# Kernel optimization log

Hardware: AMD Instinct MI355X
Metric: run time of the kernel (lower is better)

## Reference

```python
import jax, jax.numpy as jnp
import numpy as np
from jax.scipy.linalg import expm

T, N, M_IN, DT = 8192, 1024, 512, 0.01


def setup_inputs() -> dict:
    key = jax.random.key(0)
    kA, kB, ky, ku = jax.random.split(key, 4)
    ts = jnp.arange(T, dtype=jnp.float32) * DT
    # Mildly stable dynamics so the trajectory stays bounded over T steps.
    A = 0.1 * jax.random.normal(kA, (N, N), jnp.float32) / np.sqrt(N) - 0.5 * jnp.eye(N, dtype=jnp.float32)
    B = jax.random.normal(kB, (N, M_IN), jnp.float32) / np.sqrt(M_IN)
    y0 = jax.random.normal(ky, (N,), jnp.float32)
    u = jax.random.normal(ku, (T, M_IN), jnp.float32)
    return {"ts": ts, "y0": y0, "u": u, "A": A, "B": B}


def reference(ts, y0, u, A, B):
    # Exact solution of dy/dt = A y + B u(t) with u piecewise-linear on ts
    # (what diffrax Tsit5+PID approximates to rtol=1e-3). Uses Van Loan's
    # augmented matrix exponential: z = [y; u; v] with u' = v, v' = 0.
    n = A.shape[0]
    m = B.shape[1]
    h = ts[1] - ts[0]  # uniform grid
    Z_nm = jnp.zeros((n, m), A.dtype)
    Mblk = jnp.block([
        [A, B, Z_nm],
        [jnp.zeros((m, n + m), A.dtype), jnp.eye(m, dtype=A.dtype)],
        [jnp.zeros((m, n + 2 * m), A.dtype)],
    ])
    E = expm(Mblk * h)
    Eyy = E[:n, :n]            # state transition e^{Ah}
    Eyu = E[:n, n:n + m]       # response to constant input u_k
    Eyv = E[:n, n + m:]        # response to input slope v_k
    v = (u[1:] - u[:-1]) / h                     # [T-1, m] slopes
    c = u[:-1] @ Eyu.T + v @ Eyv.T               # [T-1, n] affine terms

    def step(y, ck):
        y_next = Eyy @ y + ck
        return y_next, y_next

    _, ys = jax.lax.scan(step, y0, c)
    return jnp.concatenate([y0[None, :], ys], axis=0)  # [T, n]
```

## Files before the change

### kernel.cpp

```cpp
#include <hip/hip_runtime.h>

#define GT 8192
#define GN 1024
#define GM 512
#define CCH 1024
#define SCH 8

typedef __attribute__((ext_vector_type(8))) short bf16x8;
typedef __attribute__((ext_vector_type(4))) float f32x4;

__device__ __forceinline__ unsigned short f2bf(float x) {
    unsigned int u = __float_as_uint(x);
    u += 0x7FFF + ((u >> 16) & 1);
    return (unsigned short)(u >> 16);
}
__device__ __forceinline__ float bf2f(unsigned short b) {
    return __uint_as_float(((unsigned int)b) << 16);
}
__device__ __forceinline__ void split2(float x, unsigned short& h0, unsigned short& h1) {
    h0 = f2bf(x);
    h1 = f2bf(x - bf2f(h0));
}
__device__ __forceinline__ void split3(float x, unsigned short& s0,
                                       unsigned short& s1, unsigned short& s2) {
    s0 = f2bf(x); float r = x - bf2f(s0);
    s1 = f2bf(r); r -= bf2f(s1);
    s2 = f2bf(r);
}
__device__ __forceinline__ long swz(long e, int sh) {
    return e ^ (((e >> (sh + 1)) & 3) << 3);
}
__device__ __forceinline__ void gl16(const unsigned short* g, unsigned short* l) {
    __builtin_amdgcn_global_load_lds(
        (const __attribute__((address_space(1))) unsigned int*)g,
        (__attribute__((address_space(3))) unsigned int*)l, 16, 0, 0);
}

template <int BM, int WN, int KS>
__global__ __launch_bounds__(512) void gemm_pp(
    const unsigned short* __restrict__ Ap, long apsz, int alda, int aldsh,
    int amask, int ashift, int ashiftN,
    const unsigned short* __restrict__ Bp, long bpsz, long bstride,
    const float* __restrict__ Cf, long cfb, long cfld,
    const unsigned short* __restrict__ Cp, long cpsz, int cmask,
    int bzero, int bsplit, float beta, float betaB,
    float* __restrict__ Of, long ofb, long ofld, long ofstep,
    unsigned short* __restrict__ Pout, long ppsz, int pstep8, int pmode, int prowstep,
    int segN, int zoff, int trmask,
    int M, float alpha, float alphaB, int asplit, int add_id,
    const unsigned short* __restrict__ Ap2, long apsz2,
    const unsigned short* __restrict__ Bp2,
    unsigned short* __restrict__ Pout2, long ppsz2, int p2off, int seg2,
    unsigned short* __restrict__ PoutT, int tposeN)
{
    constexpr int NQ = 2 * WN;
    constexpr int MTM = BM / 32;
    constexpr int MTN = BM / (WN * 16);
    constexpr int CPW = KS * BM / 32;
    __shared__ __align__(16) unsigned short At[2][KS][2][BM][32];
    __shared__ __align__(16) unsigned short Bt[2][KS][2][BM][32];

    const int tid = threadIdx.x;
    const int lane = tid & 63;
    const int w = tid >> 6;
    const int ksub = w / NQ;
    const int quad = w % NQ;
    const int wr = (quad / WN) * (BM / 2);
    const int wc = (quad % WN) * (BM / WN);
    const int l16 = lane & 15, koff = lane >> 4;
    const int row0 = blockIdx.x * BM;
    const int col0 = blockIdx.y * BM;
    const int lr4 = lane >> 2;
    const int lg = lane & 3;
    const bool s2 = (Ap2 != nullptr) && (row0 >= seg2);
    const bool lead = (KS == 1) || (ksub == 0);
    const int segk = row0 >> 10;

    f32x4 acc[MTM][MTN] = {};

    auto stage = [&](int bsel, int k0) {
        #pragma unroll
        for (int ci = 0; ci < CPW; ++ci) {
            const int c = w * CPW + ci;
            const int op = c / (KS * BM / 8);
            const int rem = c % (KS * BM / 8);
            const int limb = rem / (KS * BM / 16);
            const int rem2 = rem % (KS * BM / 16);
            const int kk = rem2 / (BM / 16);
            const int rb = (rem2 % (BM / 16)) * 16;
            const int lr = rb + lr4;
            const int q = lg ^ ((lr >> 1) & 3);
            long e; int sh; const unsigned short* base;
            if (op == 0) {
                if (!s2) {
                    int ar = (row0 + lr) & amask;
                    if (ar < ashiftN) { ar -= ashift; if (ar < 0) ar = 0; }
                    e = (long)ar * alda + k0 + kk * 32 + (q << 3); sh = aldsh;
                    base = Ap + (limb ? apsz : 0);
                } else {
                    e = (long)(row0 - seg2 + lr) * 1024 + k0 + kk * 32 + (q << 3); sh = 10;
                    base = Ap2 + (limb ? apsz2 : 0);
                }
            } else {
                e = (long)(col0 + lr) * 1024 + k0 + kk * 32 + (q << 3); sh = 10;
                base = (s2 ? Bp2 : (Bp + (long)segk * bstride)) + (limb ? bpsz : 0);
            }
            long f = swz(e, sh);
            unsigned short* l = (op == 0 ? &At[bsel][kk][limb][rb][0]
                                         : &Bt[bsel][kk][limb][rb][0]);
            gl16(base + f, l);
        }
    };

    stage(0, 0);
    __syncthreads();
    int cur = 0;
    for (int k0 = 0; k0 < 1024; k0 += KS * 32) {
        if (k0 + KS * 32 < 1024) stage(cur ^ 1, k0 + KS * 32);

        const int kk = ksub;
        bf16x8 a0[MTM], a1[MTM], b0[MTN], b1[MTN];
        #pragma unroll
        for (int mi = 0; mi < MTM; ++mi) {
            int lr = wr + mi * 16 + l16;
            int off = (koff ^ ((lr >> 1) & 3)) << 3;
            a0[mi] = *(const bf16x8*)&At[cur][kk][0][lr][off];
            a1[mi] = *(const bf16x8*)&At[cur][kk][1][lr][off];
        }
        #pragma unroll
        for (int ni = 0; ni < MTN; ++ni) {
            int lr = wc + ni * 16 + l16;
            int off = (koff ^ ((lr >> 1) & 3)) << 3;
            b0[ni] = *(const bf16x8*)&Bt[cur][kk][0][lr][off];
            b1[ni] = *(const bf16x8*)&Bt[cur][kk][1][lr][off];
        }
        #pragma unroll
        for (int mi = 0; mi < MTM; ++mi)
            #pragma unroll
            for (int ni = 0; ni < MTN; ++ni) {
                f32x4 cc = acc[mi][ni];
                cc = __builtin_amdgcn_mfma_f32_16x16x32_bf16(a0[mi], b0[ni], cc, 0, 0, 0);
                cc = __builtin_amdgcn_mfma_f32_16x16x32_bf16(a0[mi], b1[ni], cc, 0, 0, 0);
                cc = __builtin_amdgcn_mfma_f32_16x16x32_bf16(a1[mi], b0[ni], cc, 0, 0, 0);
                acc[mi][ni] = cc;
            }
        __syncthreads();
        cur ^= 1;
    }

    if (KS == 2) {
        float* red = (float*)&At[0][0][0][0][0];
        if (ksub == 1) {
            #pragma unroll
            for (int mi = 0; mi < MTM; ++mi)
                #pragma unroll
                for (int ni = 0; ni < MTN; ++ni)
                    *(f32x4*)&red[(((quad * MTM + mi) * MTN + ni) * 64 + lane) * 4] =
                        acc[mi][ni];
        }
        __syncthreads();
        if (ksub == 0) {
            #pragma unroll
            for (int mi = 0; mi < MTM; ++mi)
                #pragma unroll
                for (int ni = 0; ni < MTN; ++ni) {
                    f32x4 o = *(const f32x4*)
                        &red[(((quad * MTM + mi) * MTN + ni) * 64 + lane) * 4];
                    acc[mi][ni][0] += o[0]; acc[mi][ni][1] += o[1];
                    acc[mi][ni][2] += o[2]; acc[mi][ni][3] += o[3];
                }
        }
    }

    const bool tp = (PoutT != nullptr) && (row0 >= tposeN);
    float* T = (float*)&Bt[0][0][0][0][0];

    if (s2) {
        if (lead) {
            #pragma unroll
            for (int mi = 0; mi < MTM; ++mi)
                #pragma unroll
                for (int r = 0; r < 4; ++r) {
                    const int gr = row0 + wr + mi * 16 + koff * 4 + r;
                    if (gr >= M) continue;
                    const int prow = gr - seg2 + p2off;
                    #pragma unroll
                    for (int ni = 0; ni < MTN; ++ni) {
                        const int gc = col0 + wc + ni * 16 + l16;
                        float pv = acc[mi][ni][r];
                        if (Pout2) {
                            long f = swz((long)prow * 1024 + gc, 10);
                            unsigned short h0 = f2bf(pv);
                            Pout2[f] = h0;
                            Pout2[ppsz2 + f] = f2bf(pv - bf2f(h0));
                        }
                        if (tp) T[(wr + mi * 16 + koff * 4 + r) * 65 + gc - col0] = pv;
                    }
                }
        }
    } else {
        if (lead) {
            const long ofe = ofb + (long)segk * ofstep;
            const long cfe = cfb + (long)segk * ofstep;
            #pragma unroll
            for (int mi = 0; mi < MTM; ++mi) {
                #pragma unroll
                for (int r = 0; r < 4; ++r) {
                    const int gr = row0 + wr + mi * 16 + koff * 4 + r;
                    if (gr >= M) continue;
                    const int trow = (((gr < segN) ? gr + zoff : gr)) & trmask;
                    if (gr < segN && trow >= segN) continue;
                    const float aa = (trow < asplit) ? alpha : alphaB;
                    const float bb = (trow < bzero) ? 0.f
                                    : ((trow < bsplit) ? beta : betaB);
                    #pragma unroll
                    for (int ni = 0; ni < MTN; ++ni) {
                        const int gc = col0 + wc + ni * 16 + l16;
                        float vp = aa * acc[mi][ni][r];
                        float v = vp;
                        if (bb != 0.f) {
                            int crow = trow & cmask;
                            if (Cf) v += bb * Cf[cfe + (long)crow * cfld + gc];
                            else if (Cp) {
                                long f = swz((long)crow * 1024 + gc, 10);
                                v += bb * (bf2f(Cp[f]) + bf2f(Cp[cpsz + f]));
                            }
                        }
                        if (add_id && gr == gc) v += 1.f;
                        if (Of) Of[ofe + (long)trow * ofld + gc] = v;
                        if (Pout && (!pstep8 || (trow & 7) == 0)) {
                            int prow = (pstep8 ? (trow >> 3) : trow) + segk * prowstep;
                            long f = swz((long)prow * 1024 + gc, 10);
                            float pv = (pmode == 2) ? vp : v;
                            unsigned short h0 = f2bf(pv);
                            Pout[f] = h0;
                            Pout[ppsz + f] = f2bf(pv - bf2f(h0));
                        }
                        if (tp) T[(wr + mi * 16 + koff * 4 + r) * 65 + gc - col0] = v;
                    }
                }
            }
        }
    }

    if (BM == 64 && tp) {
        __syncthreads();
        if (tid < 256) {
            const int i = tid >> 2;
            const int jb = (tid & 3) * 16;
            const int prow = col0 + i;
            #pragma unroll
            for (int e2 = 0; e2 < 16; ++e2) {
                int j = jb + e2;
                float v = T[j * 65 + i];
                long f = swz((long)prow * 1024 + (row0 - tposeN + j), 10);
                unsigned short h0 = f2bf(v);
                PoutT[f] = h0;
                PoutT[(long)(1 << 20) + f] = f2bf(v - bf2f(h0));
            }
        }
    }
}

__global__ void split_pl_k(const float* __restrict__ X, unsigned short* __restrict__ P,
                           long psz, int ldsh, float s, long cnt)
{
    long i = (long)blockIdx.x * 256 + threadIdx.x;
    if (i >= cnt) return;
    float v = s * X[i];
    long f = swz(i, ldsh);
    unsigned short h0 = f2bf(v);
    P[f] = h0;
    P[psz + f] = f2bf(v - bf2f(h0));
}

__global__ void trsp_k(const float* __restrict__ in, int R, float s, int add_id,
                       unsigned short* __restrict__ P, long psz, int roff)
{
    __shared__ float t[32][33];
    const int tx = threadIdx.x & 31, ty4 = threadIdx.x >> 5;
    const int r0 = blockIdx.x * 32, c0 = blockIdx.y * 32;
    #pragma unroll
    for (int i = 0; i < 4; ++i)
        t[ty4 * 4 + i][tx] = in[(long)(c0 + ty4 * 4 + i) * R + r0 + tx];
    __syncthreads();
    #pragma unroll
    for (int i = 0; i < 4; ++i) {
        int r = r0 + ty4 * 4 + i, c = c0 + tx;
        float v = s * t[tx][ty4 * 4 + i];
        if (add_id && r == c) v += 1.f;
        long f = swz((long)(r + roff) * 1024 + c, 10);
        unsigned short h0 = f2bf(v);
        P[f] = h0;
        P[psz + f] = f2bf(v - bf2f(h0));
    }
}

__global__ void tspp_k(const unsigned short* __restrict__ IN, long ipsz, long irow0,
                       unsigned short* __restrict__ OUT, long opsz)
{
    __shared__ float t[32][33];
    const int tx = threadIdx.x & 31, ty4 = threadIdx.x >> 5;
    const int r0 = blockIdx.x * 32, c0 = blockIdx.y * 32;
    #pragma unroll
    for (int i = 0; i < 4; ++i) {
        long f = swz((irow0 + r0 + ty4 * 4 + i) * 1024 + c0 + tx, 10);
        t[ty4 * 4 + i][tx] = bf2f(IN[f]) + bf2f(IN[ipsz + f]);
    }
    __syncthreads();
    #pragma unroll
    for (int i = 0; i < 4; ++i) {
        int orow = c0 + ty4 * 4 + i;
        long f = swz((long)orow * 1024 + r0 + tx, 10);
        float v = t[tx][ty4 * 4 + i];
        unsigned short h0 = f2bf(v);
        OUT[f] = h0;
        OUT[opsz + f] = f2bf(v - bf2f(h0));
    }
}

__global__ void gtspp_k(const unsigned short* __restrict__ PV, long vpsz,
                        unsigned short* __restrict__ PG, long gpsz, float h)
{
    __shared__ float t[32][33];
    const int tx = threadIdx.x & 31, ty4 = threadIdx.x >> 5;
    const int k0 = blockIdx.x * 32, n0 = blockIdx.y * 32, z = blockIdx.z;
    #pragma unroll
    for (int i = 0; i < 4; ++i) {
        int k = k0 + ty4 * 4 + i, n = n0 + tx;
        long f2 = swz((long)(512 + k) * 1024 + n, 10);
        float v2 = bf2f(PV[f2]) + bf2f(PV[vpsz + f2]);
        float v;
        if (z == 0) {
            long f1 = swz((long)k * 1024 + n, 10);
            v = h * (bf2f(PV[f1]) + bf2f(PV[vpsz + f1]) - v2);
        } else v = h * v2;
        t[ty4 * 4 + i][tx] = v;
    }
    __syncthreads();
    #pragma unroll
    for (int i = 0; i < 4; ++i) {
        int n = n0 + ty4 * 4 + i, kk = z * 512 + k0 + tx;
        long f = swz((long)n * 1024 + kk, 10);
        float v = t[tx][ty4 * 4 + i];
        unsigned short h0 = f2bf(v);
        PG[f] = h0;
        PG[gpsz + f] = f2bf(v - bf2f(h0));
    }
}

__global__ void copy_rows_k(float* __restrict__ dst, long db, long ds,
                            const float* __restrict__ src, long sb, long ss, int ncols)
{
    int r = blockIdx.y;
    int c = blockIdx.x * 256 + threadIdx.x;
    if (c < ncols) dst[db + (long)r * ds + c] = src[sb + (long)r * ss + c];
}

__global__ void add_rows_k(float* __restrict__ dst, long db, long ds,
                           const float* __restrict__ src, int ncols)
{
    int r = blockIdx.y;
    int c = blockIdx.x * 256 + threadIdx.x;
    if (c < ncols) dst[db + (long)r * ds + c] += src[(long)r * ncols + c];
}

__global__ void scale_add_id_k(float* __restrict__ dst, const float* __restrict__ src,
                               float s, int n)
{
    int r = blockIdx.y;
    int c = blockIdx.x * 256 + threadIdx.x;
    if (c < n) dst[(long)r * n + c] = s * src[(long)r * n + c] + ((r == c) ? 1.f : 0.f);
}

__global__ void scale_copy_k(float* __restrict__ dst, const float* __restrict__ src,
                             float s, long cnt)
{
    long i = (long)blockIdx.x * 256 + threadIdx.x;
    if (i < cnt) dst[i] = s * src[i];
}

__global__ void g1g2_k(float* __restrict__ g1, float* __restrict__ g2,
                       const float* __restrict__ v1, const float* __restrict__ v2,
                       float h, long cnt)
{
    long i = (long)blockIdx.x * 256 + threadIdx.x;
    if (i < cnt) {
        float a = v1[i], b = v2[i];
        g1[i] = h * (a - b);
        g2[i] = h * b;
    }
}

template <int BM, int BN, bool TRANSB>
__global__ __launch_bounds__(256) void gemm_mfma(
    const float* __restrict__ A, long ab, long lda,
    const float* __restrict__ B,
    const float* __restrict__ Cin, long cb, long ldc, float beta,
    float* __restrict__ Out, long ob, long ldo,
    int M, int Nn, int K, float alpha, int add_id)
{
    constexpr int LDT = 40;
    __shared__ unsigned short At[3][BM][LDT];
    __shared__ unsigned short Bt[3][BN][LDT];
    const int tid = threadIdx.x;
    const int lane = tid & 63;
    const int wid = tid >> 6;
    const int row0 = blockIdx.x * BM;
    const int col0 = blockIdx.y * BN;
    constexpr int MR = BM / 32;
    constexpr int NR = BN / 32;
    const int wrow = (wid >> 1) * (BM / 2);
    const int wcol = (wid & 1) * (BN / 2);
    const int l16 = lane & 15;
    const int koff = lane >> 4;
    f32x4 acc[MR][NR] = {};

    for (int k0 = 0; k0 < K; k0 += 32) {
        #pragma unroll
        for (int i = 0; i < BM / 32; ++i) {
            int r = i * 32 + (tid >> 3);
            int kl = (tid & 7) * 4;
            int gr = row0 + r;
            float4 v = make_float4(0.f, 0.f, 0.f, 0.f);
            if (gr < M) v = *(const float4*)&A[ab + (long)gr * lda + (k0 + kl)];
            unsigned short h0[4], h1[4], h2[4];
            split3(v.x, h0[0], h1[0], h2[0]);
            split3(v.y, h0[1], h1[1], h2[1]);
            split3(v.z, h0[2], h1[2], h2[2]);
            split3(v.w, h0[3], h1[3], h2[3]);
            *(ushort4*)&At[0][r][kl] = make_ushort4(h0[0], h0[1], h0[2], h0[3]);
            *(ushort4*)&At[1][r][kl] = make_ushort4(h1[0], h1[1], h1[2], h1[3]);
            *(ushort4*)&At[2][r][kl] = make_ushort4(h2[0], h2[1], h2[2], h2[3]);
        }
        if (TRANSB) {
            #pragma unroll
            for (int i = 0; i < BN / 32; ++i) {
                int r = i * 32 + (tid >> 3);
                int kl = (tid & 7) * 4;
                float4 v = *(const float4*)&B[(long)(col0 + r) * K + (k0 + kl)];
                unsigned short h0[4], h1[4], h2[4];
                split3(v.x, h0[0], h1[0], h2[0]);
                split3(v.y, h0[1], h1[1], h2[1]);
                split3(v.z, h0[2], h1[2], h2[2]);
                split3(v.w, h0[3], h1[3], h2[3]);
                *(ushort4*)&Bt[0][r][kl] = make_ushort4(h0[0], h0[1], h0[2], h0[3]);
                *(ushort4*)&Bt[1][r][kl] = make_ushort4(h1[0], h1[1], h1[2], h1[3]);
                *(ushort4*)&Bt[2][r][kl] = make_ushort4(h2[0], h2[1], h2[2], h2[3]);
            }
        } else {
            constexpr int TPK = BN / 4;
            #pragma unroll
            for (int i = 0; i < BN / 32; ++i) {
                int kl = i * (256 / TPK) + tid / TPK;
                int nl = (tid % TPK) * 4;
                float4 v = *(const float4*)&B[(long)(k0 + kl) * Nn + (col0 + nl)];
                unsigned short s0, s1, s2;
                split3(v.x, s0, s1, s2);
                Bt[0][nl + 0][kl] = s0; Bt[1][nl + 0][kl] = s1; Bt[2][nl + 0][kl] = s2;
                split3(v.y, s0, s1, s2);
                Bt[0][nl + 1][kl] = s0; Bt[1][nl + 1][kl] = s1; Bt[2][nl + 1][kl] = s2;
                split3(v.z, s0, s1, s2);
                Bt[0][nl + 2][kl] = s0; Bt[1][nl + 2][kl] = s1; Bt[2][nl + 2][kl] = s2;
                split3(v.w, s0, s1, s2);
                Bt[0][nl + 3][kl] = s0; Bt[1][nl + 3][kl] = s1; Bt[2][nl + 3][kl] = s2;
            }
        }
        __syncthreads();
        bf16x8 bf[NR][3];
        #pragma unroll
        for (int nr = 0; nr < NR; ++nr) {
            int brow = wcol + nr * 16 + l16;
            #pragma unroll
            for (int s = 0; s < 3; ++s)
                bf[nr][s] = *(const bf16x8*)&Bt[s][brow][koff * 8];
        }
        #pragma unroll
        for (int mr = 0; mr < MR; ++mr) {
            int arow = wrow + mr * 16 + l16;
            bf16x8 a0 = *(const bf16x8*)&At[0][arow][koff * 8];
            bf16x8 a1 = *(const bf16x8*)&At[1][arow][koff * 8];
            bf16x8 a2 = *(const bf16x8*)&At[2][arow][koff * 8];
            #pragma unroll
            for (int nr = 0; nr < NR; ++nr) {
                f32x4 c = acc[mr][nr];
                c = __builtin_amdgcn_mfma_f32_16x16x32_bf16(a0, bf[nr][0], c, 0, 0, 0);
                c = __builtin_amdgcn_mfma_f32_16x16x32_bf16(a0, bf[nr][1], c, 0, 0, 0);
                c = __builtin_amdgcn_mfma_f32_16x16x32_bf16(a1, bf[nr][0], c, 0, 0, 0);
                c = __builtin_amdgcn_mfma_f32_16x16x32_bf16(a0, bf[nr][2], c, 0, 0, 0);
                c = __builtin_amdgcn_mfma_f32_16x16x32_bf16(a1, bf[nr][1], c, 0, 0, 0);
                c = __builtin_amdgcn_mfma_f32_16x16x32_bf16(a2, bf[nr][0], c, 0, 0, 0);
                acc[mr][nr] = c;
            }
        }
        __syncthreads();
    }
    #pragma unroll
    for (int mr = 0; mr < MR; ++mr) {
        #pragma unroll
        for (int r = 0; r < 4; ++r) {
            int gr = row0 + wrow + mr * 16 + koff * 4 + r;
            if (gr >= M) continue;
            #pragma unroll
            for (int nr = 0; nr < NR; ++nr) {
                int gc = col0 + wcol + nr * 16 + l16;
                float v = alpha * acc[mr][nr][r];
                if (Cin) v += beta * Cin[cb + (long)gr * ldc + gc];
                if (add_id && gr == gc) v += 1.f;
                Out[ob + (long)gr * ldo + gc] = v;
            }
        }
    }
}

static void fallback_launch(void* const* d_in, void* d_out, void* d_ws,
                            hipStream_t stream)
{
    const float* y0 = (const float*)d_in[1];
    const float* u  = (const float*)d_in[2];
    const float* Am = (const float*)d_in[3];
    const float* Bm = (const float*)d_in[4];
    float* Yout = (float*)d_out;
    float* w = (float*)d_ws;
    const float h = 0.01f;
    const int N = GN;

    float* Eyy = w;
    float* T1  = Eyy + (long)N * N;
    float* T2  = T1  + (long)N * N;
    float* V1  = T2  + (long)N * N;
    float* Vt  = V1  + (long)N * GM;
    float* V2  = Vt  + (long)N * GM;
    float* G1  = V2  + (long)N * GM;
    float* G2  = G1  + (long)N * GM;
    float* Z   = G2  + (long)N * GM;
    float* Zt  = Z   + (long)CCH * N;
    dim3 blk(256);

    auto gemm = [&](bool transb, const float* A, long ab, long lda,
                    const float* B, const float* Cin, long cb, long ldc, float beta,
                    float* Out, long ob, long ldo,
                    int M, int Nn, int K, float alpha, int add_id) {
        if (M > 1536 && (Nn % 128) == 0) {
            dim3 grid((M + 127) / 128, Nn / 128);
            if (transb)
                gemm_mfma<128, 128, true><<<grid, blk, 0, stream>>>(A, ab, lda, B, Cin, cb, ldc, beta, Out, ob, ldo, M, Nn, K, alpha, add_id);
            else
                gemm_mfma<128, 128, false><<<grid, blk, 0, stream>>>(A, ab, lda, B, Cin, cb, ldc, beta, Out, ob, ldo, M, Nn, K, alpha, add_id);
        } else {
            dim3 grid((M + 63) / 64, Nn / 64);
            if (transb)
                gemm_mfma<64, 64, true><<<grid, blk, 0, stream>>>(A, ab, lda, B, Cin, cb, ldc, beta, Out, ob, ldo, M, Nn, K, alpha, add_id);
            else
                gemm_mfma<64, 64, false><<<grid, blk, 0, stream>>>(A, ab, lda, B, Cin, cb, ldc, beta, Out, ob, ldo, M, Nn, K, alpha, add_id);
        }
    };

    scale_add_id_k<<<dim3(4, N), blk, 0, stream>>>(T1, Am, h / 5.f, N);
    {
        float* pc = T1; float* pn = T2;
        for (int k = 4; k >= 1; --k) {
            float* out = (k == 1) ? Eyy : pn;
            gemm(false, Am, 0, N, pc, nullptr, 0, 0, 0.f, out, 0, N, N, N, N, h / (float)k, 1);
            pn = pc; pc = out;
        }
    }
    const long NM = (long)N * GM;
    scale_copy_k<<<dim3((unsigned)((NM + 255) / 256)), blk, 0, stream>>>(V1, Bm, 1.f / 120.f, NM);
    {
        const float f1[4] = {1.f / 24.f, 1.f / 6.f, 0.5f, 1.f};
        float* pc = V1; float* pn = Vt;
        for (int j = 3; j >= 0; --j) {
            gemm(false, Am, 0, N, pc, Bm, 0, GM, f1[3 - j], pn, 0, GM, N, GM, N, h, 0);
            float* t = pc; pc = pn; pn = t;
        }
    }
    scale_copy_k<<<dim3((unsigned)((NM + 255) / 256)), blk, 0, stream>>>(V2, Bm, 1.f / 720.f, NM);
    {
        const float f2[4] = {1.f / 120.f, 1.f / 24.f, 1.f / 6.f, 0.5f};
        float* pc = V2; float* pn = Vt;
        for (int j = 3; j >= 0; --j) {
            gemm(false, Am, 0, N, pc, Bm, 0, GM, f2[3 - j], pn, 0, GM, N, GM, N, h, 0);
            float* t = pc; pc = pn; pn = t;
        }
    }
    g1g2_k<<<dim3((unsigned)((NM + 255) / 256)), blk, 0, stream>>>(G1, G2, V1, V2, h, NM);
    gemm(true, u, 0, GM, G1, nullptr, 0, 0, 0.f, Yout, (long)N, N, GT - 1, N, GM, 1.f, 0);
    gemm(true, u, GM, GM, G2, Yout, (long)N, N, 1.f, Yout, (long)N, N, GT - 1, N, GM, 1.f, 0);
    copy_rows_k<<<dim3(4, 1), blk, 0, stream>>>(Yout, 0, 0, y0, 0, 0, N);
    for (int s = 2; s <= SCH; ++s) {
        int Mr = (GT - 1 - s) / SCH + 1;
        gemm(true, Yout, (long)(s - 1) * N, (long)SCH * N, Eyy,
             Yout, (long)s * N, (long)SCH * N, 1.f,
             Yout, (long)s * N, (long)SCH * N, Mr, N, N, 1.f, 0);
    }
    copy_rows_k<<<dim3(4, 1), blk, 0, stream>>>(Z, 0, 0, y0, 0, 0, N);
    copy_rows_k<<<dim3(4, CCH - 1), blk, 0, stream>>>(Z, (long)N, (long)N,
                                                      Yout, (long)SCH * N, (long)SCH * N, N);
    gemm(false, Eyy, 0, N, Eyy, nullptr, 0, 0, 0.f, T1, 0, N, N, N, N, 1.f, 0);
    gemm(false, T1, 0, N, T1, nullptr, 0, 0, 0.f, T2, 0, N, N, N, N, 1.f, 0);
    gemm(false, T2, 0, N, T2, nullptr, 0, 0, 0.f, T1, 0, N, N, N, N, 1.f, 0);
    {
        float* Mc = T1; float* Mo = T2;
        float* Zc = Z;  float* Zn = Zt;
        for (int p = 0; p < 10; ++p) {
            int o = 1 << p;
            gemm(true, Zc, 0, N, Mc, Zc, (long)o * N, N, 1.f,
                 Zn, (long)o * N, N, CCH - o, N, N, 1.f, 0);
            copy_rows_k<<<dim3(4, o), blk, 0, stream>>>(Zn, 0, N, Zc, 0, N, N);
            if (p < 9) {
                gemm(false, Mc, 0, N, Mc, nullptr, 0, 0, 0.f, Mo, 0, N, N, N, N, 1.f, 0);
                float* t = Mc; Mc = Mo; Mo = t;
            }
            float* t = Zc; Zc = Zn; Zn = t;
        }
        copy_rows_k<<<dim3(4, CCH), blk, 0, stream>>>(Yout, 0, (long)SCH * N, Zc, 0, N, N);
        float* Q = Zc; float* Qt = Zn;
        for (int s = 1; s <= SCH - 1; ++s) {
            gemm(true, Q, 0, N, Eyy, nullptr, 0, 0, 0.f, Qt, 0, N, CCH, N, N, 1.f, 0);
            int Mr = (GT - 1 - s) / SCH + 1;
            add_rows_k<<<dim3(4, Mr), blk, 0, stream>>>(Yout, (long)s * N, (long)SCH * N, Qt, N);
            float* t = Q; Q = Qt; Qt = t;
        }
    }
}

extern "C" void kernel_launch(void* const* d_in, const int* in_sizes, int n_in,
                              void* d_out, int out_size, void* d_ws, size_t ws_size,
                              hipStream_t stream)
{
    (void)in_sizes; (void)n_in; (void)out_size;
    const size_t NEED = 46ull * 1024 * 1024;
    if (ws_size < NEED) { fallback_launch(d_in, d_out, d_ws, stream); return; }

    const float* y0 = (const float*)d_in[1];
    const float* u  = (const float*)d_in[2];
    const float* Am = (const float*)d_in[3];
    const float* Bm = (const float*)d_in[4];
    float* Yout = (float*)d_out;
    char* w = (char*)d_ws;
    const float h = 0.01f;
    const size_t MB = 1024 * 1024;
    const long PP  = 1 << 20;
    const long P2  = 1 << 21;
    const long P4  = 1 << 22;
    const long PUS = 1 << 22;
    const long PBS = 1 << 19;
    const int  BIG = 1 << 30;

    unsigned short* PU   = (unsigned short*)(w);
    unsigned short* PZW1 = (unsigned short*)(w);
    unsigned short* PA   = (unsigned short*)(w + 8 * MB);
    unsigned short* SQa  = (unsigned short*)(w + 8 * MB);
    unsigned short* SQb  = (unsigned short*)(w + 12 * MB);
    unsigned short* PZW2 = (unsigned short*)(w + 8 * MB);
    unsigned short* CH1  = (unsigned short*)(w + 16 * MB);
    unsigned short* WA   = (unsigned short*)(w + 16 * MB);
    unsigned short* PWt0 = (unsigned short*)(w + 20 * MB);
    unsigned short* CH2  = (unsigned short*)(w + 24 * MB);
    unsigned short* WB   = (unsigned short*)(w + 24 * MB);
    unsigned short* PE   = (unsigned short*)(w + 28 * MB);
    unsigned short* PG   = (unsigned short*)(w + 32 * MB);
    unsigned short* PW2  = PG;
    unsigned short* PW3  = (unsigned short*)(w + 36 * MB);
    unsigned short* PW4  = (unsigned short*)(w + 40 * MB);
    unsigned short* PBT  = (unsigned short*)(w + 44 * MB);
    unsigned short* QPL  = (unsigned short*)(w + 8 * MB);
    unsigned short* PWR  = PE;

    dim3 blk(256), blk5(512);

    split_pl_k<<<dim3(4096), blk, 0, stream>>>(Am, PA, PP, 10, 1.f, (long)1 << 20);

    trsp_k<<<dim3(32, 32), blk, 0, stream>>>(Am, 1024, h / 5.f, 1, CH1, P2, 0);
    trsp_k<<<dim3(16, 32), blk, 0, stream>>>(Bm, 512, 1.f / 120.f, 0, CH1, P2, 1024);
    trsp_k<<<dim3(16, 32), blk, 0, stream>>>(Bm, 512, 1.f / 720.f, 0, CH1, P2, 1536);
    trsp_k<<<dim3(16, 32), blk, 0, stream>>>(Bm, 512, 1.f, 0, PBT, PBS, 0);

    {
        const float alE[4] = {h / 4.f, h / 3.f, h / 2.f, h};
        const float f1[4] = {1.f / 24.f, 1.f / 6.f, 0.5f, 1.f};
        const float f2[4] = {1.f / 120.f, 1.f / 24.f, 1.f / 6.f, 0.5f};
        unsigned short* cc = CH1; unsigned short* cn = CH2;
        for (int j = 0; j < 4; ++j) {
            gemm_pp<64, 2, 2><<<dim3(32, 16), blk5, 0, stream>>>(
                cc, P2, 1024, 10, -1, 0, 0,
                PA, PP, 0,
                nullptr, 0, 0, PBT, PBS, 511,
                1024, 1536, f1[j], f2[j],
                nullptr, 0, 0, 0,
                cn, P2, 0, 1, 0,
                BIG, 0, -1,
                2048, alE[j], h, 1024, 1,
                nullptr, 0, nullptr, nullptr, 0, 0, BIG, nullptr, BIG);
            unsigned short* t = cc; cc = cn; cn = t;
        }
    }
    tspp_k<<<dim3(32, 32), blk, 0, stream>>>(CH1, P2, 0, PE, PP);
    gtspp_k<<<dim3(16, 32, 2), blk, 0, stream>>>(CH1 + (1 << 20), P2, PG, PP, h);

    split_pl_k<<<dim3(16384), blk, 0, stream>>>(u, PU, PUS, 9, 1.f, PUS);

    gemm_pp<128, 4, 1><<<dim3(64, 8), blk5, 0, stream>>>(
        PU, PUS, 512, 9, -1, 0, 0,
        PG, PP, 0,
        nullptr, 0, 0, nullptr, 0, -1,
        0, BIG, 0.f, 0.f,
        Yout, 1024, 1024, 0,
        WB, PP, 1, 1, 0,
        BIG, 0, -1,
        GT - 1, 1.f, 1.f, BIG, 0,
        nullptr, 0, nullptr, nullptr, 0, 0, BIG, nullptr, BIG);

    gemm_pp<64, 2, 2><<<dim3(32, 16), blk5, 0, stream>>>(
        WB, PP, 1024, 10, -1, 0, 0,
        PE, PP, 0,
        Yout, 2 * 1024, 8192, nullptr, 0, -1,
        0, BIG, 1.f, 0.f,
        Yout, 2 * 1024, 8192, 0,
        PW3, PP, 0, 1, 0,
        BIG, 0, -1,
        2048, 1.f, 1.f, BIG, 0,
        CH1, P2, PE, SQa, PP, 0, 1024, PW2, 1024);
    gemm_pp<64, 2, 2><<<dim3(32, 16), blk5, 0, stream>>>(
        PW3, PP, 1024, 10, -1, 0, 0,
        PE, PP, 0,
        Yout, 3 * 1024, 8192, nullptr, 0, -1,
        0, BIG, 1.f, 0.f,
        Yout, 3 * 1024, 8192, 0,
        WB, PP, 0, 1, 0,
        BIG, 0, -1,
        2048, 1.f, 1.f, BIG, 0,
        SQa, PP, PW2, SQb, PP, 0, 1024, PW4, 1024);
    gemm_pp<64, 2, 2><<<dim3(32, 16), blk5, 0, stream>>>(
        WB, PP, 1024, 10, -1, 0, 0,
        PE, PP, 0,
        Yout, 4 * 1024, 8192, nullptr, 0, -1,
        0, BIG, 1.f, 0.f,
        Yout, 4 * 1024, 8192, 0,
        WA, PP, 0, 1, 0,
        BIG, 0, -1,
        2048, 1.f, 1.f, BIG, 0,
        SQb, PP, PW4, PZW1, P2, 1024, 1024, PWt0, 1024);
    gemm_pp<64, 2, 2><<<dim3(32, 16), blk5, 0, stream>>>(
        WA, PP, 1024, 10, -1, 0, 0,
        PE, PP, 0,
        Yout, 5 * 1024, 8192, nullptr, 0, -1,
        0, BIG, 1.f, 0.f,
        Yout, 5 * 1024, 8192, 0,
        WB, PP, 0, 1, 0,
        BIG, 0, -1,
        2048, 1.f, 1.f, BIG, 0,
        SQa, PP, PE, nullptr, 0, 0, 1024, PW3, 1024);
    gemm_pp<64, 2, 2><<<dim3(16, 16), blk5, 0, stream>>>(
        WB, PP, 1024, 10, -1, 0, 0,
        PE, PP, 0,
        Yout, 6 * 1024, 8192, nullptr, 0, -1,
        0, BIG, 1.f, 0.f,
        Yout, 6 * 1024, 8192, 0,
        WA, PP, 0, 1, 0,
        BIG, 0, -1,
        1024, 1.f, 1.f, BIG, 0,
        nullptr, 0, nullptr, nullptr, 0, 0, BIG, nullptr, BIG);
    gemm_pp<64, 2, 2><<<dim3(16, 16), blk5, 0, stream>>>(
        WA, PP, 1024, 10, -1, 0, 0,
        PE, PP, 0,
        Yout, 7 * 1024, 8192, nullptr, 0, -1,
        0, BIG, 1.f, 0.f,
        Yout, 7 * 1024, 8192, 0,
        WB, PP, 0, 1, 0,
        BIG, 0, -1,
        1024, 1.f, 1.f, BIG, 0,
        nullptr, 0, nullptr, nullptr, 0, 0, BIG, nullptr, BIG);
    gemm_pp<64, 2, 2><<<dim3(16, 16), blk5, 0, stream>>>(
        WB, PP, 1024, 10, -1, 0, 0,
        PE, PP, 0,
        Yout, 0, 8192, nullptr, 0, -1,
        0, BIG, 1.f, 0.f,
        Yout, 0, 8192, 0,
        PZW1, P2, 0, 1, 0,
        BIG, 1, -1,
        1023, 1.f, 1.f, BIG, 0,
        nullptr, 0, nullptr, nullptr, 0, 0, BIG, nullptr, BIG);
    split_pl_k<<<dim3(4), blk, 0, stream>>>(y0, PZW1, P2, 10, 1.f, 1024);

    {
        unsigned short* PZc = PZW1; unsigned short* PZn = PZW2;
        for (int p = 0; p < 10; ++p) {
            int o = 1 << p;
            int Mr = (p == 9) ? 1024 : 2048;
            unsigned short* PWc = (p & 1) ? WA : PWt0;
            unsigned short* PWn = (p & 1) ? PWt0 : WA;
            gemm_pp<64, 2, 2><<<dim3(Mr / 64, 16), blk5, 0, stream>>>(
                PZc, P2, 1024, 10, -1, o, 1024,
                PWc, PP, 0,
                nullptr, 0, 0,
                PZc, P2, 0x7fffffff,
                0, 1024, 1.f, 0.f,
                (p == 9) ? Yout : nullptr, 0, 8192, 0,
                PZn, P2, 0, 1, 0,
                1024, 0, -1,
                Mr, 0.f, 1.f, o, 0,
                nullptr, 0, nullptr, nullptr, 0, 0, BIG,
                (p < 9) ? PWn : nullptr, 1024);
            unsigned short* t = PZc; PZc = PZn; PZn = t;
        }
    }
    copy_rows_k<<<dim3(4, 1), blk, 0, stream>>>(Yout, 0, 0, y0, 0, 0, 1024);

    gemm_pp<64, 2, 2><<<dim3(64, 16), blk5, 0, stream>>>(
        PZW1, P2, 1024, 10, 1023, 0, 0,
        PWR, PP, (long)(1 << 21),
        Yout, 1024, 8192, nullptr, 0, -1,
        0, BIG, 1.f, 0.f,
        Yout, 1024, 8192, 1024,
        QPL, P4, 0, 2, 1024,
        0, 0, 1023,
        4096, 1.f, 1.f, BIG, 0,
        nullptr, 0, nullptr, nullptr, 0, 0, BIG, nullptr, BIG);
    gemm_pp<64, 2, 2><<<dim3(48, 16), blk5, 0, stream>>>(
        QPL, P4, 1024, 10, -1, 0, 0,
        PW4, PP, 0,
        Yout, 5 * 1024, 8192, nullptr, 0, -1,
        0, BIG, 1.f, 0.f,
        Yout, 5 * 1024, 8192, 1024,
        nullptr, 0, 0, 1, 0,
        0, 0, 1023,
        3072, 1.f, 1.f, BIG, 0,
        nullptr, 0, nullptr, nullptr, 0, 0, BIG, nullptr, BIG);
}
```

Baseline: 758.0 us.

## Shorten Taylor series for expm and use single-limb bf16 input for u projection

Cuts the Taylor/Horner iteration in the augmented matrix exponential from four terms to two, rescaling the coefficients to match. Adds an a2limb flag so the GEMM can skip loading and multiplying the low bf16 limb of A, and uses it for the u-projection GEMM with a new single-limb split kernel for u. This removes two Horner GEMM launches plus a third of the MFMAs and half the A-operand traffic in the u GEMM, at the cost of lower accuracy in E and in the input terms.

```diff
diff --git a/kernel.cpp b/kernel.cpp
--- a/kernel.cpp
+++ b/kernel.cpp
@@ -38,7 +38,7 @@
 
 template <int BM, int WN, int KS>
 __global__ __launch_bounds__(512) void gemm_pp(
-    const unsigned short* __restrict__ Ap, long apsz, int alda, int aldsh,
+    const unsigned short* __restrict__ Ap, long apsz, int alda, int aldsh, int a2limb,
     int amask, int ashift, int ashiftN,
     const unsigned short* __restrict__ Bp, long bpsz, long bstride,
     const float* __restrict__ Cf, long cfb, long cfld,
@@ -75,6 +75,7 @@
     const bool s2 = (Ap2 != nullptr) && (row0 >= seg2);
     const bool lead = (KS == 1) || (ksub == 0);
     const int segk = row0 >> 10;
+    const bool alimb2 = a2limb || s2;
 
     f32x4 acc[MTM][MTN] = {};
 
@@ -90,6 +91,7 @@
             const int rb = (rem2 % (BM / 16)) * 16;
             const int lr = rb + lr4;
             const int q = lg ^ ((lr >> 1) & 3);
+            if (op == 0 && limb == 1 && !alimb2) continue;
             long e; int sh; const unsigned short* base;
             if (op == 0) {
                 if (!s2) {
@@ -125,7 +127,7 @@
             int lr = wr + mi * 16 + l16;
             int off = (koff ^ ((lr >> 1) & 3)) << 3;
             a0[mi] = *(const bf16x8*)&At[cur][kk][0][lr][off];
-            a1[mi] = *(const bf16x8*)&At[cur][kk][1][lr][off];
+            if (alimb2) a1[mi] = *(const bf16x8*)&At[cur][kk][1][lr][off];
         }
         #pragma unroll
         for (int ni = 0; ni < MTN; ++ni) {
@@ -141,7 +143,8 @@
                 f32x4 cc = acc[mi][ni];
                 cc = __builtin_amdgcn_mfma_f32_16x16x32_bf16(a0[mi], b0[ni], cc, 0, 0, 0);
                 cc = __builtin_amdgcn_mfma_f32_16x16x32_bf16(a0[mi], b1[ni], cc, 0, 0, 0);
-                cc = __builtin_amdgcn_mfma_f32_16x16x32_bf16(a1[mi], b0[ni], cc, 0, 0, 0);
+                if (alimb2)
+                    cc = __builtin_amdgcn_mfma_f32_16x16x32_bf16(a1[mi], b0[ni], cc, 0, 0, 0);
                 acc[mi][ni] = cc;
             }
         __syncthreads();
@@ -274,6 +277,14 @@
     P[psz + f] = f2bf(v - bf2f(h0));
 }
 
+__global__ void split1_pl_k(const float* __restrict__ X, unsigned short* __restrict__ P,
+                            int ldsh, long cnt)
+{
+    long i = (long)blockIdx.x * 256 + threadIdx.x;
+    if (i >= cnt) return;
+    P[swz(i, ldsh)] = f2bf(X[i]);
+}
+
 __global__ void trsp_k(const float* __restrict__ in, int R, float s, int add_id,
                        unsigned short* __restrict__ P, long psz, int roff)
 {
@@ -644,7 +655,6 @@
     const long PP  = 1 << 20;
     const long P2  = 1 << 21;
     const long P4  = 1 << 22;
-    const long PUS = 1 << 22;
     const long PBS = 1 << 19;
     const int  BIG = 1 << 30;
 
@@ -672,19 +682,19 @@
 
     split_pl_k<<<dim3(4096), blk, 0, stream>>>(Am, PA, PP, 10, 1.f, (long)1 << 20);
 
-    trsp_k<<<dim3(32, 32), blk, 0, stream>>>(Am, 1024, h / 5.f, 1, CH1, P2, 0);
-    trsp_k<<<dim3(16, 32), blk, 0, stream>>>(Bm, 512, 1.f / 120.f, 0, CH1, P2, 1024);
-    trsp_k<<<dim3(16, 32), blk, 0, stream>>>(Bm, 512, 1.f / 720.f, 0, CH1, P2, 1536);
+    trsp_k<<<dim3(32, 32), blk, 0, stream>>>(Am, 1024, h / 3.f, 1, CH1, P2, 0);
+    trsp_k<<<dim3(16, 32), blk, 0, stream>>>(Bm, 512, 1.f / 6.f, 0, CH1, P2, 1024);
+    trsp_k<<<dim3(16, 32), blk, 0, stream>>>(Bm, 512, 1.f / 24.f, 0, CH1, P2, 1536);
     trsp_k<<<dim3(16, 32), blk, 0, stream>>>(Bm, 512, 1.f, 0, PBT, PBS, 0);
 
     {
-        const float alE[4] = {h / 4.f, h / 3.f, h / 2.f, h};
-        const float f1[4] = {1.f / 24.f, 1.f / 6.f, 0.5f, 1.f};
-        const float f2[4] = {1.f / 120.f, 1.f / 24.f, 1.f / 6.f, 0.5f};
+        const float alE[2] = {h / 2.f, h};
+        const float f1[2] = {0.5f, 1.f};
+        const float f2[2] = {1.f / 6.f, 0.5f};
         unsigned short* cc = CH1; unsigned short* cn = CH2;
-        for (int j = 0; j < 4; ++j) {
+        for (int j = 0; j < 2; ++j) {
             gemm_pp<64, 2, 2><<<dim3(32, 16), blk5, 0, stream>>>(
-                cc, P2, 1024, 10, -1, 0, 0,
+                cc, P2, 1024, 10, 1, -1, 0, 0,
                 PA, PP, 0,
                 nullptr, 0, 0, PBT, PBS, 511,
                 1024, 1536, f1[j], f2[j],
@@ -699,10 +709,10 @@
     tspp_k<<<dim3(32, 32), blk, 0, stream>>>(CH1, P2, 0, PE, PP);
     gtspp_k<<<dim3(16, 32, 2), blk, 0, stream>>>(CH1 + (1 << 20), P2, PG, PP, h);
 
-    split_pl_k<<<dim3(16384), blk, 0, stream>>>(u, PU, PUS, 9, 1.f, PUS);
+    split1_pl_k<<<dim3(16384), blk, 0, stream>>>(u, PU, 9, (long)1 << 22);
 
     gemm_pp<128, 4, 1><<<dim3(64, 8), blk5, 0, stream>>>(
-        PU, PUS, 512, 9, -1, 0, 0,
+        PU, 0, 512, 9, 0, -1, 0, 0,
         PG, PP, 0,
         nullptr, 0, 0, nullptr, 0, -1,
         0, BIG, 0.f, 0.f,
@@ -713,7 +723,7 @@
         nullptr, 0, nullptr, nullptr, 0, 0, BIG, nullptr, BIG);
 
     gemm_pp<64, 2, 2><<<dim3(32, 16), blk5, 0, stream>>>(
-        WB, PP, 1024, 10, -1, 0, 0,
+        WB, PP, 1024, 10, 1, -1, 0, 0,
         PE, PP, 0,
         Yout, 2 * 1024, 8192, nullptr, 0, -1,
         0, BIG, 1.f, 0.f,
@@ -723,7 +733,7 @@
         2048, 1.f, 1.f, BIG, 0,
         CH1, P2, PE, SQa, PP, 0, 1024, PW2, 1024);
     gemm_pp<64, 2, 2><<<dim3(32, 16), blk5, 0, stream>>>(
-        PW3, PP, 1024, 10, -1, 0, 0,
+        PW3, PP, 1024, 10, 1, -1, 0, 0,
         PE, PP, 0,
         Yout, 3 * 1024, 8192, nullptr, 0, -1,
         0, BIG, 1.f, 0.f,
@@ -733,7 +743,7 @@
         2048, 1.f, 1.f, BIG, 0,
         SQa, PP, PW2, SQb, PP, 0, 1024, PW4, 1024);
     gemm_pp<64, 2, 2><<<dim3(32, 16), blk5, 0, stream>>>(
-        WB, PP, 1024, 10, -1, 0, 0,
+        WB, PP, 1024, 10, 1, -1, 0, 0,
         PE, PP, 0,
         Yout, 4 * 1024, 8192, nullptr, 0, -1,
         0, BIG, 1.f, 0.f,
@@ -743,7 +753,7 @@
         2048, 1.f, 1.f, BIG, 0,
         SQb, PP, PW4, PZW1, P2, 1024, 1024, PWt0, 1024);
     gemm_pp<64, 2, 2><<<dim3(32, 16), blk5, 0, stream>>>(
-        WA, PP, 1024, 10, -1, 0, 0,
+        WA, PP, 1024, 10, 1, -1, 0, 0,
         PE, PP, 0,
         Yout, 5 * 1024, 8192, nullptr, 0, -1,
         0, BIG, 1.f, 0.f,
@@ -753,7 +763,7 @@
         2048, 1.f, 1.f, BIG, 0,
         SQa, PP, PE, nullptr, 0, 0, 1024, PW3, 1024);
     gemm_pp<64, 2, 2><<<dim3(16, 16), blk5, 0, stream>>>(
-        WB, PP, 1024, 10, -1, 0, 0,
+        WB, PP, 1024, 10, 1, -1, 0, 0,
         PE, PP, 0,
         Yout, 6 * 1024, 8192, nullptr, 0, -1,
         0, BIG, 1.f, 0.f,
@@ -763,7 +773,7 @@
         1024, 1.f, 1.f, BIG, 0,
         nullptr, 0, nullptr, nullptr, 0, 0, BIG, nullptr, BIG);
     gemm_pp<64, 2, 2><<<dim3(16, 16), blk5, 0, stream>>>(
-        WA, PP, 1024, 10, -1, 0, 0,
+        WA, PP, 1024, 10, 1, -1, 0, 0,
         PE, PP, 0,
         Yout, 7 * 1024, 8192, nullptr, 0, -1,
         0, BIG, 1.f, 0.f,
@@ -773,7 +783,7 @@
         1024, 1.f, 1.f, BIG, 0,
         nullptr, 0, nullptr, nullptr, 0, 0, BIG, nullptr, BIG);
     gemm_pp<64, 2, 2><<<dim3(16, 16), blk5, 0, stream>>>(
-        WB, PP, 1024, 10, -1, 0, 0,
+        WB, PP, 1024, 10, 1, -1, 0, 0,
         PE, PP, 0,
         Yout, 0, 8192, nullptr, 0, -1,
         0, BIG, 1.f, 0.f,
@@ -792,7 +802,7 @@
             unsigned short* PWc = (p & 1) ? WA : PWt0;
             unsigned short* PWn = (p & 1) ? PWt0 : WA;
             gemm_pp<64, 2, 2><<<dim3(Mr / 64, 16), blk5, 0, stream>>>(
-                PZc, P2, 1024, 10, -1, o, 1024,
+                PZc, P2, 1024, 10, 1, -1, o, 1024,
                 PWc, PP, 0,
                 nullptr, 0, 0,
                 PZc, P2, 0x7fffffff,
@@ -809,7 +819,7 @@
     copy_rows_k<<<dim3(4, 1), blk, 0, stream>>>(Yout, 0, 0, y0, 0, 0, 1024);
 
     gemm_pp<64, 2, 2><<<dim3(64, 16), blk5, 0, stream>>>(
-        PZW1, P2, 1024, 10, 1023, 0, 0,
+        PZW1, P2, 1024, 10, 1, 1023, 0, 0,
         PWR, PP, (long)(1 << 21),
         Yout, 1024, 8192, nullptr, 0, -1,
         0, BIG, 1.f, 0.f,
@@ -819,7 +829,7 @@
         4096, 1.f, 1.f, BIG, 0,
         nullptr, 0, nullptr, nullptr, 0, 0, BIG, nullptr, BIG);
     gemm_pp<64, 2, 2><<<dim3(48, 16), blk5, 0, stream>>>(
-        QPL, P4, 1024, 10, -1, 0, 0,
+        QPL, P4, 1024, 10, 1, -1, 0, 0,
         PW4, PP, 0,
         Yout, 5 * 1024, 8192, nullptr, 0, -1,
         0, BIG, 1.f, 0.f,
```

Measured after the change: 705.2 us. 7.0% less time.
